# Kernel optimization log

Hardware: AMD Instinct MI355X
Metric: run time of the kernel (lower is better)

The kernel has to match this reference:

```python
import jax, jax.numpy as jnp
import numpy as np

DIM = 128
N_CENTERS = 30
CUT_LO, CUT_HI = 0.0, 10.0
N_CONV = 3
NODE_VOCAB = 100
EDGE_VOCAB = 500
N_NODES = 50000
N_EDGES = 800000
N_GRAPHS = 100
DIM_E = DIM + N_CENTERS  # 158


def setup_inputs() -> dict:
    key = jax.random.key(0)
    ks = jax.random.split(key, 20)
    def xav(k, shape):
        fan_in = shape[-2] if len(shape) >= 2 else shape[-1]
        return (jax.random.normal(k, shape, dtype=jnp.float32) / np.sqrt(fan_in)).astype(jnp.float32)
    inp = {
        'node_types': jax.random.randint(ks[0], (N_NODES,), 0, NODE_VOCAB),
        'edge_types': jax.random.randint(ks[1], (N_EDGES,), 0, EDGE_VOCAB),
        'src': jax.random.randint(ks[2], (N_EDGES,), 0, N_NODES),
        'dst': jax.random.randint(ks[3], (N_EDGES,), 0, N_NODES),
        'graph_ids': jnp.sort(jax.random.randint(ks[4], (N_NODES,), 0, N_GRAPHS)),
        'distances': jax.random.uniform(ks[5], (N_EDGES,), dtype=jnp.float32, minval=CUT_LO, maxval=CUT_HI),
        'n_graphs': N_GRAPHS,
        # embedding tables
        'node_emb': xav(ks[6], (NODE_VOCAB, DIM)),
        'edge_emb': xav(ks[7], (EDGE_VOCAB, DIM)),
        # stacked per-conv-layer weights (n_conv leading dim)
        'Wn1': xav(ks[8], (N_CONV, DIM, DIM)),  'bn1': jnp.zeros((N_CONV, DIM), jnp.float32),
        'Wn2': xav(ks[9], (N_CONV, DIM, DIM)),  'bn2': jnp.zeros((N_CONV, DIM), jnp.float32),
        'We1': xav(ks[10], (N_CONV, DIM_E, DIM)), 'be1': jnp.zeros((N_CONV, DIM), jnp.float32),
        'We2': xav(ks[11], (N_CONV, DIM, DIM)),  'be2': jnp.zeros((N_CONV, DIM), jnp.float32),
        'Wc':  xav(ks[12], (N_CONV, DIM, DIM)),  'bc': jnp.zeros((N_CONV, DIM), jnp.float32),
        # read layer
        'Wr1': xav(ks[13], (DIM, DIM)), 'br1': jnp.zeros((DIM,), jnp.float32),
        'Wr2': xav(ks[14], (DIM, 1)),   'br2': jnp.zeros((1,), jnp.float32),
    }
    return inp


def reference(node_types, edge_types, src, dst, graph_ids, distances, n_graphs,
              node_emb, edge_emb, Wn1, bn1, Wn2, bn2, We1, be1, We2, be2, Wc, bc,
              Wr1, br1, Wr2, br2):
    # embeddings
    h = node_emb[node_types]                      # [N, D]
    e_emb = edge_emb[edge_types]                  # [E, D]
    # RBF expansion of distances
    centers = jnp.linspace(CUT_LO, CUT_HI, N_CENTERS, dtype=jnp.float32)
    gap = centers[1] - centers[0]
    rbf = jnp.exp(-((distances[:, None] - centers[None, :]) ** 2) / gap)  # [E, n_centers]
    e = jnp.concatenate([e_emb, rbf], axis=1)     # [E, D + n_centers]

    n_nodes = h.shape[0]
    for i in range(N_CONV):
        node_path = jnp.maximum(h[src] @ Wn1[i] + bn1[i], 0.0) @ Wn2[i] + bn2[i]   # [E, D]
        edge_path = jnp.maximum(e @ We1[i] + be1[i], 0.0) @ We2[i] + be2[i]        # [E, D]
        m = jnp.tanh((node_path * edge_path) @ Wc[i] + bc[i])                       # [E, D]
        h = h + jax.ops.segment_sum(m, dst, num_segments=n_nodes)                   # scatter-add to dst

    # readout MLP + per-graph node sum
    hr = jnp.maximum(h @ Wr1 + br1, 0.0) @ Wr2 + br2                                # [N, 1]
    out = jax.ops.segment_sum(hr, graph_ids, num_segments=n_graphs)                 # [G, 1]
    return out.reshape(-1)
```

## Files before the change

### kernel.cpp

```cpp
#include <hip/hip_runtime.h>
#include <stdint.h>

#define NNODES 50000
#define NEDGES 800000
#define NGRAPH 100
#define NCHUNK (NEDGES / 16)
#define NWAVES 4096

typedef _Float16 f16;
typedef __attribute__((ext_vector_type(8))) _Float16 half8;
typedef __attribute__((ext_vector_type(4))) _Float16 half4;
typedef __attribute__((ext_vector_type(4))) float floatx4;

__device__ __forceinline__ void stage_WT(const float* __restrict__ W, f16* WT,
                                         int tid, int nthr) {
    for (int idx = tid; idx < 128 * 32; idx += nthr) {
        int k = idx >> 5, n4 = (idx & 31) * 4;
        floatx4 v = *(const floatx4*)(W + k * 128 + n4);
        WT[(n4 + 0) * 136 + k] = (f16)v[0];
        WT[(n4 + 1) * 136 + k] = (f16)v[1];
        WT[(n4 + 2) * 136 + k] = (f16)v[2];
        WT[(n4 + 3) * 136 + k] = (f16)v[3];
    }
}

__device__ __forceinline__ float fast_tanh(float x) {
    x = fminf(fmaxf(x, -15.0f), 15.0f);
    float e2 = __expf(2.0f * x);
    return (e2 - 1.0f) * __builtin_amdgcn_rcpf(e2 + 1.0f);
}

__device__ __forceinline__ int mtAddr(int c, int rgroup) {
    return c * 16 + ((((c >> 2) + rgroup) & 3) << 2);
}

__global__ void init_k(float* out, int osz, int* cnt) {
    int i = blockIdx.x * 256 + threadIdx.x;
    if (i < osz) out[i] = 0.0f;
    if (i < NNODES) cnt[i] = 0;
}

__global__ void hist_k(const int* __restrict__ dst, int* __restrict__ cnt) {
    int e = blockIdx.x * 256 + threadIdx.x;
    if (e < NEDGES) atomicAdd(&cnt[dst[e]], 1);
}

__global__ __launch_bounds__(1024) void scan1_k(const int* __restrict__ cnt,
                                                int* __restrict__ rowStart,
                                                int* __restrict__ blockSum) {
    __shared__ int buf[1024];
    int tid = threadIdx.x;
    int i = blockIdx.x * 1024 + tid;
    int v = (i < NNODES) ? cnt[i] : 0;
    buf[tid] = v;
    __syncthreads();
    for (int off = 1; off < 1024; off <<= 1) {
        int t = (tid >= off) ? buf[tid - off] : 0;
        __syncthreads();
        buf[tid] += t;
        __syncthreads();
    }
    if (i < NNODES) rowStart[i] = buf[tid] - v;
    if (tid == 1023) blockSum[blockIdx.x] = buf[1023];
}

__global__ void scan2_k(int* __restrict__ blockSum, int nb) {
    if (threadIdx.x == 0) {
        int run = 0;
        for (int b = 0; b < nb; ++b) { int s = blockSum[b]; blockSum[b] = run; run += s; }
    }
}

__global__ __launch_bounds__(1024) void scan3_k(int* __restrict__ rowStart,
                                                const int* __restrict__ blockSum,
                                                int* __restrict__ cnt) {
    int i = blockIdx.x * 1024 + threadIdx.x;
    if (i < NNODES) { rowStart[i] += blockSum[blockIdx.x]; cnt[i] = 0; }
    if (i == 0) rowStart[NNODES] = NEDGES;
}

__global__ void scatter_k(const int* __restrict__ src, const int* __restrict__ et,
                          const int* __restrict__ dst, const float* __restrict__ dist,
                          const int* __restrict__ rowStart, int* __restrict__ cnt,
                          uint4* __restrict__ packE) {
    int e = blockIdx.x * 256 + threadIdx.x;
    if (e >= NEDGES) return;
    int d = dst[e];
    int pos = rowStart[d] + atomicAdd(&cnt[d], 1);
    uint4 pk;
    pk.x = (unsigned)src[e];
    pk.y = (unsigned)et[e];
    pk.z = (unsigned)d;
    pk.w = __float_as_uint(dist[e]);
    packE[pos] = pk;
}

__global__ void gather_h(const int* __restrict__ nt, const float* __restrict__ emb,
                         float* __restrict__ h) {
    int i = blockIdx.x * 256 + threadIdx.x;
    int row = i >> 5, c4 = (i & 31) * 4;
    if (row < NNODES)
        *(floatx4*)(h + row * 128 + c4) = *(const floatx4*)(emb + nt[row] * 128 + c4);
}

template <int MODE>
__global__ __launch_bounds__(1024, 4) void mlp_kernel(
        const float* __restrict__ X, int M,
        const float* __restrict__ W1, const float* __restrict__ b1,
        const float* __restrict__ W2, const float* __restrict__ b2,
        f16* __restrict__ Out) {
    __shared__ f16 W1T[128 * 136];
    __shared__ f16 W2T[(MODE == 0) ? 128 * 136 : 8];
    __shared__ f16 xBuf[256 * 136];
    __shared__ float bias1[128];
    __shared__ float bias2[128];
    int tid = threadIdx.x;

    stage_WT(W1, W1T, tid, 1024);
    if (MODE == 0) stage_WT(W2, W2T, tid, 1024);
    if (tid < 128) { bias1[tid] = b1[tid]; bias2[tid] = (MODE == 0) ? b2[tid] : 0.0f; }

    int r0 = blockIdx.x * 256;
    for (int it = 0; it < 8; ++it) {
        int row = it * 32 + (tid >> 5);
        int c4 = (tid & 31) * 4;
        int gr = r0 + row;
        floatx4 x = {0.0f, 0.0f, 0.0f, 0.0f};
        if (gr < M) x = *(const floatx4*)(X + (size_t)gr * 128 + c4);
        half4 xh;
        xh[0] = (f16)x[0]; xh[1] = (f16)x[1]; xh[2] = (f16)x[2]; xh[3] = (f16)x[3];
        *(half4*)(xBuf + row * 136 + c4) = xh;
    }
    __syncthreads();

    int lane = tid & 63, wv = tid >> 6;
    int R = wv * 16;
    int n16 = lane & 15, q = lane >> 4;
    int gr = r0 + R + n16;

    half8 a[4];
    #pragma unroll
    for (int kk = 0; kk < 4; ++kk)
        a[kk] = *(const half8*)(xBuf + (R + n16) * 136 + kk * 32 + q * 8);

    #pragma unroll
    for (int f = 0; f < 8; ++f) {
        floatx4 acc = *(const floatx4*)(bias1 + f * 16 + q * 4);
        #pragma unroll
        for (int kk = 0; kk < 4; ++kk) {
            half8 aw = *(const half8*)(W1T + (f * 16 + n16) * 136 + kk * 32 + q * 8);
            acc = __builtin_amdgcn_mfma_f32_16x16x32_f16(aw, a[kk], acc, 0, 0, 0);
        }
        if (MODE == 0) {
            half4 y;
            #pragma unroll
            for (int i = 0; i < 4; ++i) y[i] = (f16)fmaxf(acc[i], 0.0f);
            *(half4*)(xBuf + (R + n16) * 136 + f * 16 + q * 4) = y;
        } else {
            half4 o;
            #pragma unroll
            for (int i = 0; i < 4; ++i) o[i] = (f16)acc[i];
            if (gr < M) *(half4*)(Out + (size_t)gr * 128 + f * 16 + q * 4) = o;
        }
    }

    if (MODE == 0) {
        #pragma unroll
        for (int kk = 0; kk < 4; ++kk)
            a[kk] = *(const half8*)(xBuf + (R + n16) * 136 + kk * 32 + q * 8);
        #pragma unroll
        for (int f = 0; f < 8; ++f) {
            floatx4 acc = *(const floatx4*)(bias2 + f * 16 + q * 4);
            #pragma unroll
            for (int kk = 0; kk < 4; ++kk) {
                half8 aw = *(const half8*)(W2T + (f * 16 + n16) * 136 + kk * 32 + q * 8);
                acc = __builtin_amdgcn_mfma_f32_16x16x32_f16(aw, a[kk], acc, 0, 0, 0);
            }
            half4 o;
            #pragma unroll
            for (int i = 0; i < 4; ++i) o[i] = (f16)acc[i];
            if (gr < M) *(half4*)(Out + (size_t)gr * 128 + f * 16 + q * 4) = o;
        }
    }
}

__global__ __launch_bounds__(1024, 4) void edge_kernel(
        const uint4* __restrict__ packE,
        const f16* __restrict__ P, const f16* __restrict__ T,
        const float* __restrict__ We1,
        const float* __restrict__ We2, const float* __restrict__ be2,
        const float* __restrict__ Wc,  const float* __restrict__ bc,
        float* __restrict__ h) {
    __shared__ f16 W2T[128 * 136];
    __shared__ f16 WcT[128 * 136];
    __shared__ f16 W1rT[128 * 40];
    __shared__ f16 Uall[16 * 2176];
    __shared__ float sbe2[128], sbc[128];
    __shared__ int dstW[16][16];

    int tid = threadIdx.x;
    stage_WT(We2, W2T, tid, 1024);
    stage_WT(Wc,  WcT, tid, 1024);
    for (int idx = tid; idx < 128 * 32; idx += 1024) {
        int n = idx >> 5, kr = idx & 31;
        W1rT[n * 40 + kr] = (kr < 30) ? (f16)We1[(128 + kr) * 128 + n] : (f16)0.0f;
    }
    if (tid < 128) { sbe2[tid] = be2[tid]; sbc[tid] = bc[tid]; }
    __syncthreads();

    int lane = tid & 63, wv = tid >> 6;
    f16* U = Uall + wv * 2176;
    int* dW = dstW[wv];
    int n16 = lane & 15, q = lane >> 4;
    const float invgap = 29.0f / 10.0f;
    int colA = lane, colB = lane + 64;
    int tsub = lane & 3, trow = lane >> 2;

    float sbcv[8];
    #pragma unroll
    for (int f = 0; f < 8; ++f) sbcv[f] = sbc[f * 16 + n16];

    int wgid = blockIdx.x * 16 + wv;
    int extra = wgid < 848 ? wgid : 848;
    int c0 = wgid * 12 + extra;
    int c1 = c0 + 12 + (wgid < 848 ? 1 : 0);

    float carry0 = 0.0f, carry1 = 0.0f;
    int prev = -1;

    uint4 pk = {0u, 0u, 0u, 0u};
    if (lane < 16) pk = packE[(size_t)c0 * 16 + lane];

    for (int ch = c0; ch < c1; ++ch) {
        bool hasNext = (ch + 1 < c1);
        int   ety  = __shfl((int)pk.y, trow);
        int   srcv = __shfl((int)pk.x, n16);
        float dcur = __shfl(__uint_as_float(pk.w), n16);
        if (lane < 16) dW[lane] = (int)pk.z;

        uint4 tr0, tr1, tr2, tr3;
        {
            const uint4* Tp = (const uint4*)(T + (size_t)ety * 128 + tsub * 32);
            tr0 = Tp[0]; tr1 = Tp[1]; tr2 = Tp[2]; tr3 = Tp[3];
        }
        half8 pA0, pA1, pA2, pA3;
        {
            const f16* Pr = P + (size_t)srcv * 128 + q * 8;
            pA0 = *(const half8*)(Pr);
            pA1 = *(const half8*)(Pr + 32);
            pA2 = *(const half8*)(Pr + 64);
            pA3 = *(const half8*)(Pr + 96);
        }
        uint4 pkn = {0u, 0u, 0u, 0u};
        if (hasNext && lane < 16) pkn = packE[(size_t)(ch + 1) * 16 + lane];

        half8 ar;
        #pragma unroll
        for (int j = 0; j < 8; ++j) {
            int k = q * 8 + j;
            float c = (float)k * (10.0f / 29.0f);
            float df = dcur - c;
            ar[j] = (f16)((k < 30) ? __expf(-df * df * invgap) : 0.0f);
        }

        {
            uint4* ub = (uint4*)(U + trow * 136 + tsub * 32);
            ub[0] = tr0; ub[1] = tr1; ub[2] = tr2; ub[3] = tr3;
        }

        #pragma unroll
        for (int f = 0; f < 8; ++f) {
            f16* up = U + n16 * 136 + f * 16 + q * 4;
            half4 tv = *(const half4*)up;
            floatx4 c4 = {(float)tv[0], (float)tv[1], (float)tv[2], (float)tv[3]};
            half8 aw = *(const half8*)(W1rT + (f * 16 + n16) * 40 + q * 8);
            c4 = __builtin_amdgcn_mfma_f32_16x16x32_f16(aw, ar, c4, 0, 0, 0);
            half4 uv;
            #pragma unroll
            for (int i = 0; i < 4; ++i) uv[i] = (f16)fmaxf(c4[i], 0.0f);
            *(half4*)up = uv;
        }

        half8 a2[4];
        #pragma unroll
        for (int kk = 0; kk < 4; ++kk)
            a2[kk] = *(const half8*)(U + n16 * 136 + kk * 32 + q * 8);
        #pragma unroll
        for (int f = 0; f < 8; ++f) {
            floatx4 acc = *(const floatx4*)(sbe2 + f * 16 + q * 4);
            #pragma unroll
            for (int kk = 0; kk < 4; ++kk) {
                half8 aw = *(const half8*)(W2T + (f * 16 + n16) * 136 + kk * 32 + q * 8);
                acc = __builtin_amdgcn_mfma_f32_16x16x32_f16(aw, a2[kk], acc, 0, 0, 0);
            }
            half4 ev;
            #pragma unroll
            for (int i = 0; i < 4; ++i) ev[i] = (f16)acc[i];
            *(half4*)(U + n16 * 136 + f * 16 + q * 4) = ev;
        }

        {
            half8 e0 = *(const half8*)(U + n16 * 136 + 0 * 32 + q * 8);
            half8 e1 = *(const half8*)(U + n16 * 136 + 1 * 32 + q * 8);
            half8 e2 = *(const half8*)(U + n16 * 136 + 2 * 32 + q * 8);
            half8 e3 = *(const half8*)(U + n16 * 136 + 3 * 32 + q * 8);
            a2[0] = e0 * pA0; a2[1] = e1 * pA1; a2[2] = e2 * pA2; a2[3] = e3 * pA3;
        }
        #pragma unroll
        for (int f = 0; f < 8; ++f) {
            float bb = sbcv[f];
            floatx4 acc = {bb, bb, bb, bb};
            #pragma unroll
            for (int kk = 0; kk < 4; ++kk) {
                half8 b = *(const half8*)(WcT + (f * 16 + n16) * 136 + kk * 32 + q * 8);
                acc = __builtin_amdgcn_mfma_f32_16x16x32_f16(a2[kk], b, acc, 0, 0, 0);
            }
            int c = f * 16 + n16;
            half4 mv;
            #pragma unroll
            for (int i = 0; i < 4; ++i) mv[i] = (f16)fast_tanh(acc[i]);
            *(half4*)(U + mtAddr(c, q)) = mv;
        }

        {
            half4 va[4], vb[4];
            #pragma unroll
            for (int g2 = 0; g2 < 4; ++g2) {
                va[g2] = *(const half4*)(U + mtAddr(colA, g2));
                vb[g2] = *(const half4*)(U + mtAddr(colB, g2));
            }
            int dArr[16];
            *(int4*)(dArr)      = *(const int4*)(dW);
            *(int4*)(dArr + 4)  = *(const int4*)(dW + 4);
            *(int4*)(dArr + 8)  = *(const int4*)(dW + 8);
            *(int4*)(dArr + 12) = *(const int4*)(dW + 12);
            #pragma unroll
            for (int r = 0; r < 16; ++r) {
                int dd = dArr[r];
                float v0 = (float)va[r >> 2][r & 3];
                float v1 = (float)vb[r >> 2][r & 3];
                if (dd != prev) {
                    if (prev >= 0) {
                        unsafeAtomicAdd(&h[(size_t)prev * 128 + colA], carry0);
                        unsafeAtomicAdd(&h[(size_t)prev * 128 + colB], carry1);
                    }
                    prev = dd; carry0 = v0; carry1 = v1;
                } else { carry0 += v0; carry1 += v1; }
            }
        }
        pk = pkn;
    }
    if (prev >= 0) {
        unsafeAtomicAdd(&h[(size_t)prev * 128 + colA], carry0);
        unsafeAtomicAdd(&h[(size_t)prev * 128 + colB], carry1);
    }
}

__global__ __launch_bounds__(1024, 4) void readout_k(
        const float* __restrict__ X, int M,
        const float* __restrict__ W1, const float* __restrict__ b1,
        const float* __restrict__ Wr2, const float* __restrict__ br2,
        const int* __restrict__ gid, float* __restrict__ out) {
    __shared__ f16 W1T[128 * 136];
    __shared__ f16 xBuf[256 * 136];
    __shared__ float bias1[128];
    __shared__ float sWr2[128];
    int tid = threadIdx.x;

    stage_WT(W1, W1T, tid, 1024);
    if (tid < 128) { bias1[tid] = b1[tid]; sWr2[tid] = Wr2[tid]; }

    int r0 = blockIdx.x * 256;
    for (int it = 0; it < 8; ++it) {
        int row = it * 32 + (tid >> 5);
        int c4 = (tid & 31) * 4;
        int gr = r0 + row;
        floatx4 x = {0.0f, 0.0f, 0.0f, 0.0f};
        if (gr < M) x = *(const floatx4*)(X + (size_t)gr * 128 + c4);
        half4 xh;
        xh[0] = (f16)x[0]; xh[1] = (f16)x[1]; xh[2] = (f16)x[2]; xh[3] = (f16)x[3];
        *(half4*)(xBuf + row * 136 + c4) = xh;
    }
    __syncthreads();

    int lane = tid & 63, wv = tid >> 6;
    int R = wv * 16;
    int n16 = lane & 15, q = lane >> 4;

    half8 a[4];
    #pragma unroll
    for (int kk = 0; kk < 4; ++kk)
        a[kk] = *(const half8*)(xBuf + (R + n16) * 136 + kk * 32 + q * 8);

    floatx4 acc[8];
    #pragma unroll
    for (int f = 0; f < 8; ++f) {
        float bb = bias1[f * 16 + n16];
        acc[f] = (floatx4){bb, bb, bb, bb};
        #pragma unroll
        for (int kk = 0; kk < 4; ++kk) {
            half8 b = *(const half8*)(W1T + (f * 16 + n16) * 136 + kk * 32 + q * 8);
            acc[f] = __builtin_amdgcn_mfma_f32_16x16x32_f16(a[kk], b, acc[f], 0, 0, 0);
        }
    }

    float s[4];
    #pragma unroll
    for (int i = 0; i < 4; ++i) {
        float t = 0.0f;
        #pragma unroll
        for (int f = 0; f < 8; ++f)
            t += fmaxf(acc[f][i], 0.0f) * sWr2[f * 16 + n16];
        #pragma unroll
        for (int m = 1; m < 16; m <<= 1) t += __shfl_xor(t, m);
        s[i] = t;
    }

    if (n16 == 0) {
        float br2v = br2[0];
        float t = 0.0f; int g = -1;
        #pragma unroll
        for (int i = 0; i < 4; ++i) {
            int gr = r0 + R + q * 4 + i;
            if (gr < M) {
                int gi = gid[gr];
                float si = s[i] + br2v;
                if (gi == g) t += si;
                else { if (g >= 0) unsafeAtomicAdd(&out[g], t); g = gi; t = si; }
            }
        }
        if (g >= 0) unsafeAtomicAdd(&out[g], t);
    }
}

extern "C" void kernel_launch(void* const* d_in, const int* in_sizes, int n_in,
                              void* d_out, int out_size, void* d_ws, size_t ws_size,
                              hipStream_t stream) {
    (void)in_sizes; (void)n_in; (void)ws_size;
    const int*   node_types = (const int*)d_in[0];
    const int*   edge_types = (const int*)d_in[1];
    const int*   src        = (const int*)d_in[2];
    const int*   dst        = (const int*)d_in[3];
    const int*   graph_ids  = (const int*)d_in[4];
    const float* distances  = (const float*)d_in[5];
    const float* node_emb   = (const float*)d_in[7];
    const float* edge_emb   = (const float*)d_in[8];
    const float* Wn1 = (const float*)d_in[9];
    const float* bn1 = (const float*)d_in[10];
    const float* Wn2 = (const float*)d_in[11];
    const float* bn2 = (const float*)d_in[12];
    const float* We1 = (const float*)d_in[13];
    const float* be1 = (const float*)d_in[14];
    const float* We2 = (const float*)d_in[15];
    const float* be2 = (const float*)d_in[16];
    const float* Wc  = (const float*)d_in[17];
    const float* bc  = (const float*)d_in[18];
    const float* Wr1 = (const float*)d_in[19];
    const float* br1 = (const float*)d_in[20];
    const float* Wr2 = (const float*)d_in[21];
    const float* br2 = (const float*)d_in[22];

    char* w = (char*)d_ws;
    auto carve = [&](size_t bytes) { char* p = w; w += (bytes + 255) & ~(size_t)255; return p; };
    float* h        = (float*)carve((size_t)NNODES * 128 * 4);
    f16*   P        = (f16*)  carve((size_t)NNODES * 128 * 2);
    f16*   T        = (f16*)  carve((size_t)500 * 128 * 2);
    int*   rowStart = (int*)  carve((size_t)(NNODES + 1) * 4);
    int*   cnt      = (int*)  carve((size_t)NNODES * 4);
    int*   blockSum = (int*)  carve((size_t)64 * 4);
    uint4* packE    = (uint4*)carve((size_t)NEDGES * 16);

    float* out = (float*)d_out;
    const int NB1 = (NNODES + 1023) / 1024;

    init_k<<<(NNODES + 255) / 256, 256, 0, stream>>>(out, out_size, cnt);
    hist_k<<<NEDGES / 256, 256, 0, stream>>>(dst, cnt);
    scan1_k<<<NB1, 1024, 0, stream>>>(cnt, rowStart, blockSum);
    scan2_k<<<1, 64, 0, stream>>>(blockSum, NB1);
    scan3_k<<<NB1, 1024, 0, stream>>>(rowStart, blockSum, cnt);
    scatter_k<<<NEDGES / 256, 256, 0, stream>>>(src, edge_types, dst, distances,
                                                rowStart, cnt, packE);
    gather_h<<<(NNODES * 32 + 255) / 256, 256, 0, stream>>>(node_types, node_emb, h);

    for (int i = 0; i < 3; ++i) {
        mlp_kernel<2><<<(500 + 255) / 256, 1024, 0, stream>>>(
            edge_emb, 500, We1 + (size_t)i * 158 * 128, be1 + i * 128, nullptr, nullptr, T);
        mlp_kernel<0><<<(NNODES + 255) / 256, 1024, 0, stream>>>(
            h, NNODES, Wn1 + (size_t)i * 128 * 128, bn1 + i * 128,
            Wn2 + (size_t)i * 128 * 128, bn2 + i * 128, P);
        edge_kernel<<<256, 1024, 0, stream>>>(
            packE, P, T,
            We1 + (size_t)i * 158 * 128,
            We2 + (size_t)i * 128 * 128, be2 + i * 128,
            Wc + (size_t)i * 128 * 128, bc + i * 128, h);
    }

    readout_k<<<(NNODES + 255) / 256, 1024, 0, stream>>>(
        h, NNODES, Wr1, br1, Wr2, br2, graph_ids, out);
}
```

Measured before the change: 781.3 us.

## Process two 16-edge tiles per wave iteration in edge kernel

The edge kernel now handles 32 edges per chunk as two 16-row MFMA tiles. Each weight fragment loaded from LDS is reused by two MFMAs, and more independent work is in flight to hide latency. Edge-type rows are loaded straight into registers instead of being staged through LDS, and dst indices come from shuffles rather than a shared array. The scatter-add writes columns in two halves of 64 lanes over 32 rows. The cost is higher register pressure, which could reduce occupancy or cause spills at 1024 threads per block.

```diff
diff --git a/kernel.cpp b/kernel.cpp
--- a/kernel.cpp
+++ b/kernel.cpp
@@ -4,7 +4,7 @@
 #define NNODES 50000
 #define NEDGES 800000
 #define NGRAPH 100
-#define NCHUNK (NEDGES / 16)
+#define NCH32 (NEDGES / 32)
 #define NWAVES 4096
 
 typedef _Float16 f16;
@@ -28,10 +28,6 @@
     x = fminf(fmaxf(x, -15.0f), 15.0f);
     float e2 = __expf(2.0f * x);
     return (e2 - 1.0f) * __builtin_amdgcn_rcpf(e2 + 1.0f);
-}
-
-__device__ __forceinline__ int mtAddr(int c, int rgroup) {
-    return c * 16 + ((((c >> 2) + rgroup) & 3) << 2);
 }
 
 __global__ void init_k(float* out, int osz, int* cnt) {
@@ -196,7 +192,6 @@
     __shared__ f16 W1rT[128 * 40];
     __shared__ f16 Uall[16 * 2176];
     __shared__ float sbe2[128], sbc[128];
-    __shared__ int dstW[16][16];
 
     int tid = threadIdx.x;
     stage_WT(We2, W2T, tid, 1024);
@@ -210,149 +205,184 @@
 
     int lane = tid & 63, wv = tid >> 6;
     f16* U = Uall + wv * 2176;
-    int* dW = dstW[wv];
     int n16 = lane & 15, q = lane >> 4;
     const float invgap = 29.0f / 10.0f;
-    int colA = lane, colB = lane + 64;
-    int tsub = lane & 3, trow = lane >> 2;
 
     float sbcv[8];
     #pragma unroll
     for (int f = 0; f < 8; ++f) sbcv[f] = sbc[f * 16 + n16];
 
     int wgid = blockIdx.x * 16 + wv;
-    int extra = wgid < 848 ? wgid : 848;
-    int c0 = wgid * 12 + extra;
-    int c1 = c0 + 12 + (wgid < 848 ? 1 : 0);
-
-    float carry0 = 0.0f, carry1 = 0.0f;
+    int extra = wgid < 424 ? wgid : 424;
+    int c0 = wgid * 6 + extra;
+    int c1 = c0 + 6 + (wgid < 424 ? 1 : 0);
+
+    float carryA = 0.0f, carryB = 0.0f;
     int prev = -1;
 
     uint4 pk = {0u, 0u, 0u, 0u};
-    if (lane < 16) pk = packE[(size_t)c0 * 16 + lane];
+    if (lane < 32) pk = packE[(size_t)c0 * 32 + lane];
 
     for (int ch = c0; ch < c1; ++ch) {
-        bool hasNext = (ch + 1 < c1);
-        int   ety  = __shfl((int)pk.y, trow);
-        int   srcv = __shfl((int)pk.x, n16);
-        float dcur = __shfl(__uint_as_float(pk.w), n16);
-        if (lane < 16) dW[lane] = (int)pk.z;
-
-        uint4 tr0, tr1, tr2, tr3;
+        uint4 pkn = {0u, 0u, 0u, 0u};
+        if (ch + 1 < c1 && lane < 32) pkn = packE[(size_t)(ch + 1) * 32 + lane];
+
+        int   ety0 = __shfl((int)pk.y, n16);
+        int   ety1 = __shfl((int)pk.y, 16 + n16);
+        int   src0 = __shfl((int)pk.x, n16);
+        int   src1 = __shfl((int)pk.x, 16 + n16);
+        float d0   = __shfl(__uint_as_float(pk.w), n16);
+        float d1   = __shfl(__uint_as_float(pk.w), 16 + n16);
+
+        half4 t0[8], t1[8];
         {
-            const uint4* Tp = (const uint4*)(T + (size_t)ety * 128 + tsub * 32);
-            tr0 = Tp[0]; tr1 = Tp[1]; tr2 = Tp[2]; tr3 = Tp[3];
-        }
-        half8 pA0, pA1, pA2, pA3;
-        {
-            const f16* Pr = P + (size_t)srcv * 128 + q * 8;
-            pA0 = *(const half8*)(Pr);
-            pA1 = *(const half8*)(Pr + 32);
-            pA2 = *(const half8*)(Pr + 64);
-            pA3 = *(const half8*)(Pr + 96);
-        }
-        uint4 pkn = {0u, 0u, 0u, 0u};
-        if (hasNext && lane < 16) pkn = packE[(size_t)(ch + 1) * 16 + lane];
-
-        half8 ar;
+            const f16* Tp0 = T + (size_t)ety0 * 128 + q * 4;
+            const f16* Tp1 = T + (size_t)ety1 * 128 + q * 4;
+            #pragma unroll
+            for (int f = 0; f < 8; ++f) {
+                t0[f] = *(const half4*)(Tp0 + f * 16);
+                t1[f] = *(const half4*)(Tp1 + f * 16);
+            }
+        }
+
+        half8 ar0, ar1;
         #pragma unroll
         for (int j = 0; j < 8; ++j) {
             int k = q * 8 + j;
             float c = (float)k * (10.0f / 29.0f);
-            float df = dcur - c;
-            ar[j] = (f16)((k < 30) ? __expf(-df * df * invgap) : 0.0f);
-        }
-
-        {
-            uint4* ub = (uint4*)(U + trow * 136 + tsub * 32);
-            ub[0] = tr0; ub[1] = tr1; ub[2] = tr2; ub[3] = tr3;
-        }
-
+            float df0 = d0 - c, df1 = d1 - c;
+            ar0[j] = (f16)((k < 30) ? __expf(-df0 * df0 * invgap) : 0.0f);
+            ar1[j] = (f16)((k < 30) ? __expf(-df1 * df1 * invgap) : 0.0f);
+        }
+
+        half8 a20[4], a21[4];
         #pragma unroll
         for (int f = 0; f < 8; ++f) {
-            f16* up = U + n16 * 136 + f * 16 + q * 4;
-            half4 tv = *(const half4*)up;
+            half4 tv = t0[f];
             floatx4 c4 = {(float)tv[0], (float)tv[1], (float)tv[2], (float)tv[3]};
             half8 aw = *(const half8*)(W1rT + (f * 16 + n16) * 40 + q * 8);
-            c4 = __builtin_amdgcn_mfma_f32_16x16x32_f16(aw, ar, c4, 0, 0, 0);
+            c4 = __builtin_amdgcn_mfma_f32_16x16x32_f16(aw, ar0, c4, 0, 0, 0);
             half4 uv;
             #pragma unroll
             for (int i = 0; i < 4; ++i) uv[i] = (f16)fmaxf(c4[i], 0.0f);
-            *(half4*)up = uv;
-        }
-
-        half8 a2[4];
+            *(half4*)(U + n16 * 136 + f * 16 + q * 4) = uv;
+        }
         #pragma unroll
         for (int kk = 0; kk < 4; ++kk)
-            a2[kk] = *(const half8*)(U + n16 * 136 + kk * 32 + q * 8);
+            a20[kk] = *(const half8*)(U + n16 * 136 + kk * 32 + q * 8);
+
         #pragma unroll
         for (int f = 0; f < 8; ++f) {
-            floatx4 acc = *(const floatx4*)(sbe2 + f * 16 + q * 4);
+            half4 tv = t1[f];
+            floatx4 c4 = {(float)tv[0], (float)tv[1], (float)tv[2], (float)tv[3]};
+            half8 aw = *(const half8*)(W1rT + (f * 16 + n16) * 40 + q * 8);
+            c4 = __builtin_amdgcn_mfma_f32_16x16x32_f16(aw, ar1, c4, 0, 0, 0);
+            half4 uv;
+            #pragma unroll
+            for (int i = 0; i < 4; ++i) uv[i] = (f16)fmaxf(c4[i], 0.0f);
+            *(half4*)(U + n16 * 136 + f * 16 + q * 4) = uv;
+        }
+        #pragma unroll
+        for (int kk = 0; kk < 4; ++kk)
+            a21[kk] = *(const half8*)(U + n16 * 136 + kk * 32 + q * 8);
+
+        half8 pA0[4], pA1[4];
+        {
+            const f16* Pr0 = P + (size_t)src0 * 128 + q * 8;
+            const f16* Pr1 = P + (size_t)src1 * 128 + q * 8;
+            #pragma unroll
+            for (int kk = 0; kk < 4; ++kk) {
+                pA0[kk] = *(const half8*)(Pr0 + kk * 32);
+                pA1[kk] = *(const half8*)(Pr1 + kk * 32);
+            }
+        }
+
+        half4 ep1r[8];
+        #pragma unroll
+        for (int f = 0; f < 8; ++f) {
+            floatx4 acc0 = *(const floatx4*)(sbe2 + f * 16 + q * 4);
+            floatx4 acc1 = acc0;
             #pragma unroll
             for (int kk = 0; kk < 4; ++kk) {
                 half8 aw = *(const half8*)(W2T + (f * 16 + n16) * 136 + kk * 32 + q * 8);
-                acc = __builtin_amdgcn_mfma_f32_16x16x32_f16(aw, a2[kk], acc, 0, 0, 0);
-            }
-            half4 ev;
-            #pragma unroll
-            for (int i = 0; i < 4; ++i) ev[i] = (f16)acc[i];
-            *(half4*)(U + n16 * 136 + f * 16 + q * 4) = ev;
-        }
-
-        {
-            half8 e0 = *(const half8*)(U + n16 * 136 + 0 * 32 + q * 8);
-            half8 e1 = *(const half8*)(U + n16 * 136 + 1 * 32 + q * 8);
-            half8 e2 = *(const half8*)(U + n16 * 136 + 2 * 32 + q * 8);
-            half8 e3 = *(const half8*)(U + n16 * 136 + 3 * 32 + q * 8);
-            a2[0] = e0 * pA0; a2[1] = e1 * pA1; a2[2] = e2 * pA2; a2[3] = e3 * pA3;
-        }
-        #pragma unroll
-        for (int f = 0; f < 8; ++f) {
-            float bb = sbcv[f];
-            floatx4 acc = {bb, bb, bb, bb};
-            #pragma unroll
-            for (int kk = 0; kk < 4; ++kk) {
-                half8 b = *(const half8*)(WcT + (f * 16 + n16) * 136 + kk * 32 + q * 8);
-                acc = __builtin_amdgcn_mfma_f32_16x16x32_f16(a2[kk], b, acc, 0, 0, 0);
-            }
-            int c = f * 16 + n16;
-            half4 mv;
-            #pragma unroll
-            for (int i = 0; i < 4; ++i) mv[i] = (f16)fast_tanh(acc[i]);
-            *(half4*)(U + mtAddr(c, q)) = mv;
-        }
-
-        {
-            half4 va[4], vb[4];
-            #pragma unroll
-            for (int g2 = 0; g2 < 4; ++g2) {
-                va[g2] = *(const half4*)(U + mtAddr(colA, g2));
-                vb[g2] = *(const half4*)(U + mtAddr(colB, g2));
-            }
-            int dArr[16];
-            *(int4*)(dArr)      = *(const int4*)(dW);
-            *(int4*)(dArr + 4)  = *(const int4*)(dW + 4);
-            *(int4*)(dArr + 8)  = *(const int4*)(dW + 8);
-            *(int4*)(dArr + 12) = *(const int4*)(dW + 12);
-            #pragma unroll
-            for (int r = 0; r < 16; ++r) {
-                int dd = dArr[r];
-                float v0 = (float)va[r >> 2][r & 3];
-                float v1 = (float)vb[r >> 2][r & 3];
-                if (dd != prev) {
-                    if (prev >= 0) {
-                        unsafeAtomicAdd(&h[(size_t)prev * 128 + colA], carry0);
-                        unsafeAtomicAdd(&h[(size_t)prev * 128 + colB], carry1);
-                    }
-                    prev = dd; carry0 = v0; carry1 = v1;
-                } else { carry0 += v0; carry1 += v1; }
-            }
-        }
+                acc0 = __builtin_amdgcn_mfma_f32_16x16x32_f16(aw, a20[kk], acc0, 0, 0, 0);
+                acc1 = __builtin_amdgcn_mfma_f32_16x16x32_f16(aw, a21[kk], acc1, 0, 0, 0);
+            }
+            half4 e0;
+            #pragma unroll
+            for (int i = 0; i < 4; ++i) e0[i] = (f16)acc0[i];
+            *(half4*)(U + n16 * 136 + f * 16 + q * 4) = e0;
+            half4 e1;
+            #pragma unroll
+            for (int i = 0; i < 4; ++i) e1[i] = (f16)acc1[i];
+            ep1r[f] = e1;
+        }
+
+        half8 a2e0[4], a2e1[4];
+        #pragma unroll
+        for (int kk = 0; kk < 4; ++kk) {
+            half8 e = *(const half8*)(U + n16 * 136 + kk * 32 + q * 8);
+            a2e0[kk] = e * pA0[kk];
+        }
+        #pragma unroll
+        for (int f = 0; f < 8; ++f)
+            *(half4*)(U + n16 * 136 + f * 16 + q * 4) = ep1r[f];
+        #pragma unroll
+        for (int kk = 0; kk < 4; ++kk) {
+            half8 e = *(const half8*)(U + n16 * 136 + kk * 32 + q * 8);
+            a2e1[kk] = e * pA1[kk];
+        }
+
+        int prevIn = prev;
+        int prevOut = prev;
+        #pragma unroll
+        for (int p = 0; p < 2; ++p) {
+            #pragma unroll
+            for (int fo = 0; fo < 4; ++fo) {
+                int f = p * 4 + fo;
+                float bb = sbcv[f];
+                floatx4 acc0 = {bb, bb, bb, bb};
+                floatx4 acc1 = {bb, bb, bb, bb};
+                #pragma unroll
+                for (int kk = 0; kk < 4; ++kk) {
+                    half8 bw = *(const half8*)(WcT + (f * 16 + n16) * 136 + kk * 32 + q * 8);
+                    acc0 = __builtin_amdgcn_mfma_f32_16x16x32_f16(a2e0[kk], bw, acc0, 0, 0, 0);
+                    acc1 = __builtin_amdgcn_mfma_f32_16x16x32_f16(a2e1[kk], bw, acc1, 0, 0, 0);
+                }
+                int cs = fo * 16 + n16;
+                half4 m0, m1;
+                #pragma unroll
+                for (int i = 0; i < 4; ++i) { m0[i] = (f16)fast_tanh(acc0[i]); m1[i] = (f16)fast_tanh(acc1[i]); }
+                *(half4*)(U + cs * 32 + ((((cs >> 2) + q) & 7) << 2)) = m0;
+                *(half4*)(U + cs * 32 + ((((cs >> 2) + 4 + q) & 7) << 2)) = m1;
+            }
+            {
+                half4 v[8];
+                #pragma unroll
+                for (int rg = 0; rg < 8; ++rg)
+                    v[rg] = *(const half4*)(U + lane * 32 + ((((lane >> 2) + rg) & 7) << 2));
+                float cr = (p == 0) ? carryA : carryB;
+                int pv = prevIn;
+                float* hc = h + (size_t)p * 64 + lane;
+                #pragma unroll
+                for (int r = 0; r < 32; ++r) {
+                    int dd = __shfl((int)pk.z, r);
+                    float val = (float)v[r >> 2][r & 3];
+                    if (dd != pv) {
+                        if (pv >= 0) unsafeAtomicAdd(hc + (size_t)pv * 128, cr);
+                        pv = dd; cr = val;
+                    } else cr += val;
+                }
+                if (p == 0) carryA = cr; else carryB = cr;
+                prevOut = pv;
+            }
+        }
+        prev = prevOut;
         pk = pkn;
     }
     if (prev >= 0) {
-        unsafeAtomicAdd(&h[(size_t)prev * 128 + colA], carry0);
-        unsafeAtomicAdd(&h[(size_t)prev * 128 + colB], carry1);
+        unsafeAtomicAdd(&h[(size_t)prev * 128 + lane], carryA);
+        unsafeAtomicAdd(&h[(size_t)prev * 128 + 64 + lane], carryB);
     }
 }
 
```

Measured after the change: 1.271 ms. 62.7% more time.
